# Kernel optimization log

Measured on AMD Instinct MI355X. Metric: run time of the kernel, lower is better.

## Reference

```python
import jax, jax.numpy as jnp
import numpy as np

EMBED_DIM = 1024
NUM_HEADS = 16
HEAD_DIM = EMBED_DIM // NUM_HEADS


def setup_inputs() -> dict:
    key = jax.random.key(0)
    ks = jax.random.split(key, 6)
    B, S, D = 2, 2048, EMBED_DIM
    scale = 1.0 / np.sqrt(D)
    return {
        "inputs": jax.random.normal(ks[0], (B, S, D), dtype=jnp.float32),
        "Wq": jax.random.normal(ks[1], (D, D), dtype=jnp.float32) * scale,
        "Wk": jax.random.normal(ks[2], (D, D), dtype=jnp.float32) * scale,
        "Wv": jax.random.normal(ks[3], (D, D), dtype=jnp.float32) * scale,
        "Wo": jax.random.normal(ks[4], (D, D), dtype=jnp.float32) * scale,
        "bo": jnp.zeros((D,), dtype=jnp.float32),
    }


def reference(inputs, Wq, Wk, Wv, Wo, bo):
    B, S, D = inputs.shape
    H, P = NUM_HEADS, HEAD_DIM
    # torch Linear: x @ W.T ; weights stored [out, in]
    q = inputs @ Wq.T
    k = inputs @ Wk.T
    v = inputs @ Wv.T
    # separate heads: [B, S, H, P] -> [B, H, S, P]
    q = q.reshape(B, S, H, P).transpose(0, 2, 1, 3)
    k = k.reshape(B, S, H, P).transpose(0, 2, 1, 3)
    v = v.reshape(B, S, H, P).transpose(0, 2, 1, 3)
    # scaled dot-product attention; scale = 1/sqrt(P + 1e-9)
    scale = 1.0 / jnp.sqrt(jnp.float32(P) + 1e-9)
    scores = jnp.einsum("bhsp,bhtp->bhst", q, k) * scale
    weights = jax.nn.softmax(scores, axis=-1)
    attn = jnp.einsum("bhst,bhtp->bhsp", weights, v)
    # merge heads -> [B, S, D]
    concat = attn.transpose(0, 2, 1, 3).reshape(B, S, D)
    return concat @ Wo.T + bo
```

## Files before the change

### kernel.cpp

```cpp
#include <hip/hip_runtime.h>
#include <hip/hip_bf16.h>

typedef __bf16 bf16;
typedef __bf16 bf16x4 __attribute__((ext_vector_type(4)));
typedef __bf16 bf16x8 __attribute__((ext_vector_type(8)));
typedef short  s16x4  __attribute__((ext_vector_type(4)));
typedef float  f32x4  __attribute__((ext_vector_type(4)));

#define QSCALE 0.18033688011112042f

__device__ __forceinline__ float exp2_raw(float x) {
    return __builtin_amdgcn_exp2f(x);
}

__device__ __forceinline__ void load16_lds(const bf16* g, bf16* l) {
    __builtin_amdgcn_global_load_lds(
        (const __attribute__((address_space(1))) unsigned int*)g,
        (__attribute__((address_space(3))) unsigned int*)l, 16, 0, 0);
}

__global__ void cvt_f32_bf16(
    const float* __restrict__ s0, const float* __restrict__ s1,
    const float* __restrict__ s2, const float* __restrict__ s3,
    const float* __restrict__ s4,
    bf16* __restrict__ d0, bf16* __restrict__ d1, bf16* __restrict__ d2,
    bf16* __restrict__ d3, bf16* __restrict__ d4)
{
    const float* s; bf16* d; int nblk;
    switch (blockIdx.y) {
        case 0:  s = s0; d = d0; nblk = 2048; break;
        case 1:  s = s1; d = d1; nblk = 512;  break;
        case 2:  s = s2; d = d2; nblk = 512;  break;
        case 3:  s = s3; d = d3; nblk = 512;  break;
        default: s = s4; d = d4; nblk = 512;  break;
    }
    if ((int)blockIdx.x >= nblk) return;
    int idx = blockIdx.x * 256 + threadIdx.x;
    float4 a = ((const float4*)s)[idx * 2];
    float4 b = ((const float4*)s)[idx * 2 + 1];
    bf16x8 o;
    o[0] = (bf16)a.x; o[1] = (bf16)a.y; o[2] = (bf16)a.z; o[3] = (bf16)a.w;
    o[4] = (bf16)b.x; o[5] = (bf16)b.y; o[6] = (bf16)b.z; o[7] = (bf16)b.w;
    *(bf16x8*)&d[idx * 8] = o;
}

__global__ __launch_bounds__(256, 2) void qkv_gemm(
    const bf16* __restrict__ A,
    const bf16* __restrict__ Wq, const bf16* __restrict__ Wk,
    const bf16* __restrict__ Wv,
    bf16* __restrict__ qbuf, bf16* __restrict__ kbuf, bf16* __restrict__ vT)
{
    __shared__ bf16 sA[128 * 32];
    __shared__ bf16 sB[128 * 32];

    const int hwflat = blockIdx.y * 24 + blockIdx.x;
    const int xcd    = hwflat & 7;
    const int slot   = hwflat >> 3;
    const int my     = xcd * 4 + slot / 24;
    const int mx     = slot % 24;

    const int which = mx >> 3;
    const int n0    = (mx & 7) * 128;
    const int m0    = my * 128;
    const bf16* B   = (which == 0) ? Wq : (which == 1) ? Wk : Wv;

    const int tid  = threadIdx.x;
    const int lane = tid & 63;
    const int w    = tid >> 6;
    const int wr   = w >> 1, wc = w & 1;
    const int r    = lane & 15;
    const int qd   = lane >> 4;

    f32x4 acc[4][4];
    const f32x4 zero4 = {0.f, 0.f, 0.f, 0.f};
#pragma unroll
    for (int mi = 0; mi < 4; ++mi)
#pragma unroll
        for (int ni = 0; ni < 4; ++ni) acc[mi][ni] = zero4;

    for (int kt = 0; kt < 32; ++kt) {
        const bf16* gA = A + (size_t)m0 * 1024 + kt * 32;
        const bf16* gB = B + (size_t)n0 * 1024 + kt * 32;
        __syncthreads();
#pragma unroll
        for (int j = 0; j < 2; ++j) {
            int task = j * 256 + tid;
            int row  = task >> 2, ch = task & 3;
            int ldsb = (j * 256 + w * 64) * 8;
            load16_lds(gA + (size_t)row * 1024 + ch * 8, &sA[ldsb]);
            load16_lds(gB + (size_t)row * 1024 + ch * 8, &sB[ldsb]);
        }
        __syncthreads();

        bf16x8 af[4], bfr[4];
#pragma unroll
        for (int mi = 0; mi < 4; ++mi)
            af[mi] = *(const bf16x8*)&sA[(wr * 64 + mi * 16 + r) * 32 + qd * 8];
#pragma unroll
        for (int ni = 0; ni < 4; ++ni)
            bfr[ni] = *(const bf16x8*)&sB[(wc * 64 + ni * 16 + r) * 32 + qd * 8];
#pragma unroll
        for (int mi = 0; mi < 4; ++mi)
#pragma unroll
            for (int ni = 0; ni < 4; ++ni)
                acc[mi][ni] = __builtin_amdgcn_mfma_f32_16x16x32_bf16(
                    af[mi], bfr[ni], acc[mi][ni], 0, 0, 0);
    }

    const float scale = (which == 0) ? QSCALE : 1.0f;
#pragma unroll
    for (int mi = 0; mi < 4; ++mi)
#pragma unroll
        for (int ni = 0; ni < 4; ++ni) {
            int rb  = m0 + wr * 64 + mi * 16 + qd * 4;
            int col = n0 + wc * 64 + ni * 16 + r;
            if (which == 2) {
                bf16x4 pv;
#pragma unroll
                for (int i = 0; i < 4; ++i) pv[i] = (bf16)acc[mi][ni][i];
                *(bf16x4*)&vT[((size_t)((rb >> 11) * 1024 + col)) * 2048 + (rb & 2047)] = pv;
            } else {
                bf16* dst = (which == 0) ? qbuf : kbuf;
#pragma unroll
                for (int i = 0; i < 4; ++i)
                    dst[(size_t)(rb + i) * 1024 + col] = (bf16)(acc[mi][ni][i] * scale);
            }
        }
}

__global__ __launch_bounds__(256, 2) void out_gemm(
    const bf16* __restrict__ A, const bf16* __restrict__ B,
    float* __restrict__ C, const float* __restrict__ bias)
{
    __shared__ bf16 sA[128 * 32];
    __shared__ bf16 sB[64 * 32];

    const int hwflat = blockIdx.y * 16 + blockIdx.x;
    const int xcd    = hwflat & 7;
    const int slot   = hwflat >> 3;
    const int m0     = (xcd * 4 + (slot >> 4)) * 128;
    const int n0     = (slot & 15) * 64;

    const int tid  = threadIdx.x;
    const int lane = tid & 63;
    const int w    = tid >> 6;
    const int wr   = w >> 1, wc = w & 1;
    const int r    = lane & 15;
    const int qd   = lane >> 4;

    f32x4 acc[4][2];
    const f32x4 zero4 = {0.f, 0.f, 0.f, 0.f};
#pragma unroll
    for (int mi = 0; mi < 4; ++mi)
#pragma unroll
        for (int ni = 0; ni < 2; ++ni) acc[mi][ni] = zero4;

    for (int kt = 0; kt < 32; ++kt) {
        const bf16* gA = A + (size_t)m0 * 1024 + kt * 32;
        const bf16* gB = B + (size_t)n0 * 1024 + kt * 32;
        __syncthreads();
#pragma unroll
        for (int j = 0; j < 2; ++j) {
            int task = j * 256 + tid;
            int row  = task >> 2, ch = task & 3;
            int ldsb = (j * 256 + w * 64) * 8;
            load16_lds(gA + (size_t)row * 1024 + ch * 8, &sA[ldsb]);
        }
        {
            int row = tid >> 2, ch = tid & 3;
            int ldsb = (w * 64) * 8;
            load16_lds(gB + (size_t)row * 1024 + ch * 8, &sB[ldsb]);
        }
        __syncthreads();

        bf16x8 af[4], bfr[2];
#pragma unroll
        for (int mi = 0; mi < 4; ++mi)
            af[mi] = *(const bf16x8*)&sA[(wr * 64 + mi * 16 + r) * 32 + qd * 8];
#pragma unroll
        for (int ni = 0; ni < 2; ++ni)
            bfr[ni] = *(const bf16x8*)&sB[(wc * 32 + ni * 16 + r) * 32 + qd * 8];
#pragma unroll
        for (int mi = 0; mi < 4; ++mi)
#pragma unroll
            for (int ni = 0; ni < 2; ++ni)
                acc[mi][ni] = __builtin_amdgcn_mfma_f32_16x16x32_bf16(
                    af[mi], bfr[ni], acc[mi][ni], 0, 0, 0);
    }

#pragma unroll
    for (int mi = 0; mi < 4; ++mi)
#pragma unroll
        for (int ni = 0; ni < 2; ++ni)
#pragma unroll
            for (int i = 0; i < 4; ++i) {
                int row = m0 + wr * 64 + mi * 16 + qd * 4 + i;
                int col = n0 + wc * 32 + ni * 16 + r;
                C[(size_t)row * 1024 + col] = acc[mi][ni][i] + bias[col];
            }
}

__global__ __launch_bounds__(512, 4) void attn_kernel(
    const bf16* __restrict__ qbuf, const bf16* __restrict__ kbuf,
    const bf16* __restrict__ vT, bf16* __restrict__ concat)
{
    __shared__ bf16 sKV[8 * 64 * 72];

    const int tid  = threadIdx.x;
    const int lane = tid & 63;
    const int w    = tid >> 6;
    const int g    = w >> 2;
    const int wq   = w & 3;
    const int gtid = tid & 255;
    const int r    = lane & 15;
    const int qd   = lane >> 4;

    const int hwflat = blockIdx.y * 16 + blockIdx.x;
    const int xcd    = hwflat & 7;
    const int slot   = hwflat >> 3;
    const int bh     = xcd * 4 + (slot >> 4);
    const int qt     = slot & 15;

    const int b    = bh >> 4, h = bh & 15;
    const int qrow0 = b * 2048 + qt * 128;
    const size_t vbase = (size_t)bh * 64 * 2048;

    const s16x4 ones4 = {(short)0x3F80, (short)0x3F80, (short)0x3F80, (short)0x3F80};

    int krow[2], kch[2];
#pragma unroll
    for (int t = 0; t < 2; ++t) {
        int flat = t * 256 + gtid;
        krow[t] = flat >> 3; kch[t] = flat & 7;
    }

    bf16x8 aq[2][2];
#pragma unroll
    for (int mi = 0; mi < 2; ++mi)
#pragma unroll
        for (int ks = 0; ks < 2; ++ks)
            aq[mi][ks] = *(const bf16x8*)&qbuf[
                (size_t)(qrow0 + wq * 32 + mi * 16 + r) * 1024 + h * 64 + ks * 32 + qd * 8];

    f32x4 acc_o[2][4], acc_l[2];
    const f32x4 zero4 = {0.f, 0.f, 0.f, 0.f};
#pragma unroll
    for (int mi = 0; mi < 2; ++mi) {
        acc_l[mi] = zero4;
#pragma unroll
        for (int pj = 0; pj < 4; ++pj) acc_o[mi][pj] = zero4;
    }

    bf16* const myKV = &sKV[g * 4 * 4608];

    bf16x8 rk[2], rv[2];
#pragma unroll
    for (int t = 0; t < 2; ++t) {
        rk[t] = *(const bf16x8*)&kbuf[(size_t)(b * 2048 + g * 64 + krow[t]) * 1024 + h * 64 + kch[t] * 8];
        rv[t] = *(const bf16x8*)&vT[vbase + (size_t)krow[t] * 2048 + g * 64 + kch[t] * 8];
    }
#pragma unroll
    for (int t = 0; t < 2; ++t) {
        *(bf16x8*)&myKV[0 * 4608 + krow[t] * 72 + kch[t] * 8] = rk[t];
        *(bf16x8*)&myKV[1 * 4608 + krow[t] * 72 + kch[t] * 8] = rv[t];
    }
#pragma unroll
    for (int t = 0; t < 2; ++t) {
        rk[t] = *(const bf16x8*)&kbuf[(size_t)(b * 2048 + (2 + g) * 64 + krow[t]) * 1024 + h * 64 + kch[t] * 8];
        rv[t] = *(const bf16x8*)&vT[vbase + (size_t)krow[t] * 2048 + (2 + g) * 64 + kch[t] * 8];
    }
    __syncthreads();

    for (int tt = 0; tt < 16; ++tt) {
        {
            int st = (tt + 1) & 1;
#pragma unroll
            for (int t = 0; t < 2; ++t) {
                *(bf16x8*)&myKV[(2 * st + 0) * 4608 + krow[t] * 72 + kch[t] * 8] = rk[t];
                *(bf16x8*)&myKV[(2 * st + 1) * 4608 + krow[t] * 72 + kch[t] * 8] = rv[t];
            }
        }
        {
            int nxtl = (tt + 2 < 16) ? tt + 2 : 15;
            int gt   = 2 * nxtl + g;
#pragma unroll
            for (int t = 0; t < 2; ++t) {
                rk[t] = *(const bf16x8*)&kbuf[(size_t)(b * 2048 + gt * 64 + krow[t]) * 1024 + h * 64 + kch[t] * 8];
                rv[t] = *(const bf16x8*)&vT[vbase + (size_t)krow[t] * 2048 + gt * 64 + kch[t] * 8];
            }
        }
        const bf16* sK = &myKV[(2 * (tt & 1) + 0) * 4608];
        const bf16* sV = &myKV[(2 * (tt & 1) + 1) * 4608];

        f32x4 accs[2][4];
#pragma unroll
        for (int mi = 0; mi < 2; ++mi)
#pragma unroll
            for (int ni = 0; ni < 4; ++ni) accs[mi][ni] = zero4;
        __builtin_amdgcn_s_setprio(1);
#pragma unroll
        for (int ks = 0; ks < 2; ++ks)
#pragma unroll
            for (int ni = 0; ni < 4; ++ni) {
                bf16x8 ak = *(const bf16x8*)&sK[(ni * 16 + r) * 72 + ks * 32 + qd * 8];
#pragma unroll
                for (int mi = 0; mi < 2; ++mi)
                    accs[mi][ni] = __builtin_amdgcn_mfma_f32_16x16x32_bf16(
                        ak, aq[mi][ks], accs[mi][ni], 0, 0, 0);
            }
        __builtin_amdgcn_s_setprio(0);

        s16x4 pfrag[2][4];
#pragma unroll
        for (int mi = 0; mi < 2; ++mi)
#pragma unroll
            for (int ni = 0; ni < 4; ++ni) {
                bf16x4 pv;
#pragma unroll
                for (int i = 0; i < 4; ++i) pv[i] = (bf16)exp2_raw(accs[mi][ni][i]);
                pfrag[mi][ni] = __builtin_bit_cast(s16x4, pv);
            }

        __builtin_amdgcn_s_setprio(1);
#pragma unroll
        for (int ni = 0; ni < 4; ++ni) {
#pragma unroll
            for (int pj = 0; pj < 4; ++pj) {
                bf16x4 av = *(const bf16x4*)&sV[(pj * 16 + r) * 72 + ni * 16 + qd * 4];
                s16x4  avs = __builtin_bit_cast(s16x4, av);
#pragma unroll
                for (int mi = 0; mi < 2; ++mi)
                    acc_o[mi][pj] = __builtin_amdgcn_mfma_f32_16x16x16bf16_1k(
                        avs, pfrag[mi][ni], acc_o[mi][pj], 0, 0, 0);
            }
#pragma unroll
            for (int mi = 0; mi < 2; ++mi)
                acc_l[mi] = __builtin_amdgcn_mfma_f32_16x16x16bf16_1k(
                    ones4, pfrag[mi][ni], acc_l[mi], 0, 0, 0);
        }
        __builtin_amdgcn_s_setprio(0);

        __syncthreads();
    }

    float* sF = (float*)sKV;
    bf16*  sO = sKV + 18432;

    if (g == 1) {
        int slotc = gtid * 35;
#pragma unroll
        for (int mi = 0; mi < 2; ++mi)
#pragma unroll
            for (int pj = 0; pj < 4; ++pj)
#pragma unroll
                for (int i = 0; i < 4; ++i)
                    sF[slotc + mi * 16 + pj * 4 + i] = acc_o[mi][pj][i];
        sF[slotc + 32] = acc_l[0][0];
        sF[slotc + 33] = acc_l[1][0];
    }
    __syncthreads();
    if (g == 0) {
        int slotc = gtid * 35;
        float inv[2];
#pragma unroll
        for (int mi = 0; mi < 2; ++mi)
            inv[mi] = 1.0f / (acc_l[mi][0] + sF[slotc + 32 + mi]);
#pragma unroll
        for (int mi = 0; mi < 2; ++mi) {
            int qloc = wq * 32 + mi * 16 + r;
#pragma unroll
            for (int pj = 0; pj < 4; ++pj)
#pragma unroll
                for (int i = 0; i < 4; ++i) {
                    float o = acc_o[mi][pj][i] + sF[slotc + mi * 16 + pj * 4 + i];
                    sO[qloc * 72 + pj * 16 + qd * 4 + i] = (bf16)(o * inv[mi]);
                }
        }
    }
    __syncthreads();
    {
        int row = tid >> 2;
        int q4  = tid & 3;
        size_t cb = (size_t)(qrow0 + row) * 1024 + h * 64 + q4 * 16;
        *(bf16x8*)&concat[cb]     = *(const bf16x8*)&sO[row * 72 + q4 * 16];
        *(bf16x8*)&concat[cb + 8] = *(const bf16x8*)&sO[row * 72 + q4 * 16 + 8];
    }
}

extern "C" void kernel_launch(void* const* d_in, const int* in_sizes, int n_in,
                              void* d_out, int out_size, void* d_ws, size_t ws_size,
                              hipStream_t stream)
{
    const float* x  = (const float*)d_in[0];
    const float* Wq = (const float*)d_in[1];
    const float* Wk = (const float*)d_in[2];
    const float* Wv = (const float*)d_in[3];
    const float* Wo = (const float*)d_in[4];
    const float* bo = (const float*)d_in[5];
    float* out = (float*)d_out;

    char* ws = (char*)d_ws;
    bf16* xb     = (bf16*)(ws);
    bf16* Wqb    = (bf16*)(ws + (8u  << 20));
    bf16* Wkb    = (bf16*)(ws + (10u << 20));
    bf16* Wvb    = (bf16*)(ws + (12u << 20));
    bf16* Wob    = (bf16*)(ws + (14u << 20));
    bf16* qbuf   = (bf16*)(ws + (16u << 20));
    bf16* kbuf   = (bf16*)(ws + (24u << 20));
    bf16* vT     = (bf16*)(ws + (32u << 20));
    bf16* concat = (bf16*)(ws + (40u << 20));

    hipLaunchKernelGGL(cvt_f32_bf16, dim3(2048, 5), dim3(256), 0, stream,
                       x, Wq, Wk, Wv, Wo, xb, Wqb, Wkb, Wvb, Wob);
    hipLaunchKernelGGL(qkv_gemm, dim3(24, 32), dim3(256), 0, stream,
                       xb, Wqb, Wkb, Wvb, qbuf, kbuf, vT);
    hipLaunchKernelGGL(attn_kernel, dim3(16, 32), dim3(512), 0, stream,
                       qbuf, kbuf, vT, concat);
    hipLaunchKernelGGL(out_gemm, dim3(16, 32), dim3(256), 0, stream,
                       concat, Wob, out, bo);
}
```

Baseline: 188.0 us.

## Software-pipeline attention loop so PV of previous tile overlaps QK of current

Restructures the KV loop so each iteration runs the QK MFMAs for tile t together with the PV MFMAs for tile t-1, whose probabilities were computed in the prior step. The exp2 conversion then happens after both matmuls, and a final PV epilogue drains the last tile. Register double-buffering (A/B prefetch sets) lets the loop be unrolled by two without copying. The goal is to hide exp latency behind matrix work. In exchange it adds an extra barrier per iteration and raises register pressure.

Result: slower. 259.3 us (+37.9%).

```diff
diff --git a/kernel.cpp b/kernel.cpp
--- a/kernel.cpp
+++ b/kernel.cpp
@@ -253,44 +253,39 @@
 
     bf16* const myKV = &sKV[g * 4 * 4608];
 
-    bf16x8 rk[2], rv[2];
+    bf16x8 rkA[2], rvA[2], rkB[2], rvB[2];
+    s16x4 pfrag[2][4];
+
 #pragma unroll
     for (int t = 0; t < 2; ++t) {
-        rk[t] = *(const bf16x8*)&kbuf[(size_t)(b * 2048 + g * 64 + krow[t]) * 1024 + h * 64 + kch[t] * 8];
-        rv[t] = *(const bf16x8*)&vT[vbase + (size_t)krow[t] * 2048 + g * 64 + kch[t] * 8];
+        rkA[t] = *(const bf16x8*)&kbuf[(size_t)(b * 2048 + g * 64 + krow[t]) * 1024 + h * 64 + kch[t] * 8];
+        rvA[t] = *(const bf16x8*)&vT[vbase + (size_t)krow[t] * 2048 + g * 64 + kch[t] * 8];
     }
 #pragma unroll
     for (int t = 0; t < 2; ++t) {
-        *(bf16x8*)&myKV[0 * 4608 + krow[t] * 72 + kch[t] * 8] = rk[t];
-        *(bf16x8*)&myKV[1 * 4608 + krow[t] * 72 + kch[t] * 8] = rv[t];
+        *(bf16x8*)&myKV[0 * 4608 + krow[t] * 72 + kch[t] * 8] = rkA[t];
+        *(bf16x8*)&myKV[1 * 4608 + krow[t] * 72 + kch[t] * 8] = rvA[t];
     }
 #pragma unroll
     for (int t = 0; t < 2; ++t) {
-        rk[t] = *(const bf16x8*)&kbuf[(size_t)(b * 2048 + (2 + g) * 64 + krow[t]) * 1024 + h * 64 + kch[t] * 8];
-        rv[t] = *(const bf16x8*)&vT[vbase + (size_t)krow[t] * 2048 + (2 + g) * 64 + kch[t] * 8];
+        rkA[t] = *(const bf16x8*)&kbuf[(size_t)(b * 2048 + (2 + g) * 64 + krow[t]) * 1024 + h * 64 + kch[t] * 8];
+        rvA[t] = *(const bf16x8*)&vT[vbase + (size_t)krow[t] * 2048 + (2 + g) * 64 + kch[t] * 8];
     }
     __syncthreads();
 
-    for (int tt = 0; tt < 16; ++tt) {
-        {
-            int st = (tt + 1) & 1;
-#pragma unroll
-            for (int t = 0; t < 2; ++t) {
-                *(bf16x8*)&myKV[(2 * st + 0) * 4608 + krow[t] * 72 + kch[t] * 8] = rk[t];
-                *(bf16x8*)&myKV[(2 * st + 1) * 4608 + krow[t] * 72 + kch[t] * 8] = rv[t];
-            }
-        }
+    auto subiter = [&](int tt, bf16x8 (&rkW)[2], bf16x8 (&rvW)[2],
+                       bf16x8 (&rkL)[2], bf16x8 (&rvL)[2], bool doPV) {
         {
             int nxtl = (tt + 2 < 16) ? tt + 2 : 15;
             int gt   = 2 * nxtl + g;
 #pragma unroll
             for (int t = 0; t < 2; ++t) {
-                rk[t] = *(const bf16x8*)&kbuf[(size_t)(b * 2048 + gt * 64 + krow[t]) * 1024 + h * 64 + kch[t] * 8];
-                rv[t] = *(const bf16x8*)&vT[vbase + (size_t)krow[t] * 2048 + gt * 64 + kch[t] * 8];
-            }
-        }
-        const bf16* sK = &myKV[(2 * (tt & 1) + 0) * 4608];
-        const bf16* sV = &myKV[(2 * (tt & 1) + 1) * 4608];
+                rkL[t] = *(const bf16x8*)&kbuf[(size_t)(b * 2048 + gt * 64 + krow[t]) * 1024 + h * 64 + kch[t] * 8];
+                rvL[t] = *(const bf16x8*)&vT[vbase + (size_t)krow[t] * 2048 + gt * 64 + kch[t] * 8];
+            }
+        }
+        const bf16* sK  = &myKV[(2 * (tt & 1) + 0) * 4608];
+        const bf16* sVp = &myKV[(2 * ((tt & 1) ^ 1) + 1) * 4608];
 
         f32x4 accs[2][4];
 #pragma unroll
@@ -308,9 +303,27 @@
                     accs[mi][ni] = __builtin_amdgcn_mfma_f32_16x16x32_bf16(
                         ak, aq[mi][ks], accs[mi][ni], 0, 0, 0);
             }
+
+        if (doPV) {
+#pragma unroll
+            for (int ni = 0; ni < 4; ++ni) {
+#pragma unroll
+                for (int pj = 0; pj < 4; ++pj) {
+                    bf16x4 av = *(const bf16x4*)&sVp[(pj * 16 + r) * 72 + ni * 16 + qd * 4];
+                    s16x4  avs = __builtin_bit_cast(s16x4, av);
+#pragma unroll
+                    for (int mi = 0; mi < 2; ++mi)
+                        acc_o[mi][pj] = __builtin_amdgcn_mfma_f32_16x16x16bf16_1k(
+                            avs, pfrag[mi][ni], acc_o[mi][pj], 0, 0, 0);
+                }
+#pragma unroll
+                for (int mi = 0; mi < 2; ++mi)
+                    acc_l[mi] = __builtin_amdgcn_mfma_f32_16x16x16bf16_1k(
+                        ones4, pfrag[mi][ni], acc_l[mi], 0, 0, 0);
+            }
+        }
         __builtin_amdgcn_s_setprio(0);
 
-        s16x4 pfrag[2][4];
 #pragma unroll
         for (int mi = 0; mi < 2; ++mi)
 #pragma unroll
@@ -321,6 +334,24 @@
                 pfrag[mi][ni] = __builtin_bit_cast(s16x4, pv);
             }
 
+        __syncthreads();
+
+#pragma unroll
+        for (int t = 0; t < 2; ++t) {
+            *(bf16x8*)&myKV[(2 * ((tt + 1) & 1) + 0) * 4608 + krow[t] * 72 + kch[t] * 8] = rkW[t];
+            *(bf16x8*)&myKV[(2 * ((tt + 1) & 1) + 1) * 4608 + krow[t] * 72 + kch[t] * 8] = rvW[t];
+        }
+
+        __syncthreads();
+    };
+
+    for (int tt2 = 0; tt2 < 16; tt2 += 2) {
+        subiter(tt2,     rkA, rvA, rkB, rvB, tt2 != 0);
+        subiter(tt2 + 1, rkB, rvB, rkA, rvA, true);
+    }
+
+    {
+        const bf16* sV = &myKV[(2 * 1 + 1) * 4608];
         __builtin_amdgcn_s_setprio(1);
 #pragma unroll
         for (int ni = 0; ni < 4; ++ni) {
@@ -339,9 +370,8 @@
                     ones4, pfrag[mi][ni], acc_l[mi], 0, 0, 0);
         }
         __builtin_amdgcn_s_setprio(0);
-
-        __syncthreads();
-    }
+    }
+    __syncthreads();
 
     float* sF = (float*)sKV;
     bf16*  sO = sKV + 18432;
```
